# Performance work log

Measured on AMD Instinct MI355X. Metric: run time of the kernel, lower is better.

The kernel has to match this reference:

```python
import jax, jax.numpy as jnp
import numpy as np

B, S, H = 16, 2048, 1024

def setup_inputs() -> dict:
    key = jax.random.key(0)
    ks = jax.random.split(key, 6)
    return {
        "h": jax.random.normal(ks[0], (1, B, H), jnp.float32),
        "c": jax.random.normal(ks[1], (1, B, H), jnp.float32),
        "encoder_outputs": jax.random.normal(ks[2], (B, S, H), jnp.float32),
        "attn_W": jax.random.normal(ks[3], (H, 2 * H), jnp.float32) * 0.02,
        "attn_b": jax.random.normal(ks[4], (H,), jnp.float32) * 0.02,
        "v_W": jax.random.normal(ks[5], (1, H), jnp.float32) * 0.02,
    }

def reference(h, c, encoder_outputs, attn_W, attn_b, v_W):
    # h: (1,B,H) -> (B,1,H); a: (B,S,H)
    a = encoder_outputs
    hq = jnp.transpose(h, (1, 0, 2))  # (B,1,H)
    # cat((s, a), -1) @ attn_W.T == s @ Wh.T + a @ Wa.T (avoids (B,S,2H) buffer)
    Wh, Wa = attn_W[:, :H], attn_W[:, H:]
    energy = jax.nn.relu(
        jnp.einsum("bqh,oh->bqo", hq, Wh)          # (B,1,H), broadcast over S
        + jnp.einsum("bsh,oh->bso", a, Wa)
        + attn_b
    )  # (B,S,H)
    scores = jnp.einsum("bsh,h->bs", energy, v_W[0])  # (B,S)
    attn_weights = jax.nn.softmax(scores, axis=1)      # (B,S)
    context = jnp.einsum("bs,bsh->bh", attn_weights, a)[:, None, :]  # (B,1,H)
    return context, attn_weights
```

## Files before the change

kernel.cpp:

```cpp
#include <hip/hip_runtime.h>
#include <hip/hip_bf16.h>


typedef __bf16 bf16x8 __attribute__((ext_vector_type(8)));
typedef float floatx4 __attribute__((ext_vector_type(4)));

#define BB 16
#define SS 2048
#define HH 1024
#define MM (BB * SS)

#define GLB(p) ((const __attribute__((address_space(1))) void*)(p))
#define LDSP(p) ((__attribute__((address_space(3))) void*)(p))

__device__ inline ushort f2bf(float x) {
    uint32_t u = __builtin_bit_cast(uint32_t, x);
    u += 0x7FFFu + ((u >> 16) & 1u);
    return (ushort)(u >> 16);
}

__global__ __launch_bounds__(256) void convert_A_kernel(
    const float* __restrict__ src, __bf16* __restrict__ dst)
{
    size_t i = (size_t)blockIdx.x * 256 + threadIdx.x;
    const float* s = src + i * 8;
    float4 a = *(const float4*)(s);
    float4 b = *(const float4*)(s + 4);
    union { ushort u[8]; uint4 v; } p;
    p.u[0] = f2bf(a.x); p.u[1] = f2bf(a.y); p.u[2] = f2bf(a.z); p.u[3] = f2bf(a.w);
    p.u[4] = f2bf(b.x); p.u[5] = f2bf(b.y); p.u[6] = f2bf(b.z); p.u[7] = f2bf(b.w);
    *(uint4*)(dst + i * 8) = p.v;
}

__global__ __launch_bounds__(256) void prep_kernel(
    const float* __restrict__ h, const float* __restrict__ W,
    const float* __restrict__ bias, float* __restrict__ projh,
    __bf16* __restrict__ Wb, float* __restrict__ scores, float* __restrict__ ctx)
{
    int bid = blockIdx.x;
    int tid = threadIdx.x;
    if (bid < 256) {
        int b = bid >> 4;
        int oc = bid & 15;
        __shared__ float hrow[HH];
        *(float4*)&hrow[tid * 4] = *(const float4*)(h + (size_t)b * HH + tid * 4);
        __syncthreads();
        int ol = tid >> 2;
        int kq = tid & 3;
        int o = oc * 64 + ol;
        const float* wr = W + (size_t)o * (2 * HH) + kq * 256;
        const float* hb = hrow + kq * 256;
        float sum = 0.f;
        for (int k = 0; k < 256; k += 4) {
            float4 wv = *(const float4*)(wr + k);
            sum += hb[k] * wv.x + hb[k + 1] * wv.y + hb[k + 2] * wv.z + hb[k + 3] * wv.w;
        }
        sum += __shfl_xor(sum, 1);
        sum += __shfl_xor(sum, 2);
        if (kq == 0) projh[b * HH + o] = sum + bias[o];
    } else if (bid < 320) {
        int cb = bid - 256;
#pragma unroll
        for (int j = 0; j < 8; j++) {
            int g = cb * 2048 + tid + j * 256;
            int o = g >> 7;
            int k = (g & 127) * 8;
            const float* s = W + (size_t)o * (2 * HH) + HH + k;
            float4 a = *(const float4*)(s);
            float4 b2 = *(const float4*)(s + 4);
            union { ushort u[8]; uint4 v; } p;
            p.u[0] = f2bf(a.x); p.u[1] = f2bf(a.y); p.u[2] = f2bf(a.z); p.u[3] = f2bf(a.w);
            p.u[4] = f2bf(b2.x); p.u[5] = f2bf(b2.y); p.u[6] = f2bf(b2.z); p.u[7] = f2bf(b2.w);
            *(uint4*)(Wb + (size_t)o * HH + k) = p.v;
        }
    } else {
        int zb = bid - 320;
        float4 z = make_float4(0.f, 0.f, 0.f, 0.f);
        float* sp = scores + zb * 2048 + tid * 8;
        *(float4*)(sp) = z;
        *(float4*)(sp + 4) = z;
        *(float4*)(ctx + zb * 1024 + tid * 4) = z;
    }
}

__global__ __launch_bounds__(256) void gemm_scores_kernel(
    const __bf16* __restrict__ Ab,
    const __bf16* __restrict__ Wb,
    const float* __restrict__ projh,
    const float* __restrict__ vW,
    float* __restrict__ scores)
{
    constexpr int BM = 128, BN = 128, BK = 32;

    __shared__ __bf16 As[BM * BK];
    __shared__ __bf16 Bs[BN * BK];

    const int bid = blockIdx.x;
    const int grp = bid >> 6;
    const int r   = bid & 63;
    const int n0 = (r >> 3) * BN;
    const int my = grp * 8 + (r & 7);
    const int m0 = my * BM;
    const int bidx = m0 >> 11;

    const int tid = threadIdx.x;
    const int lane = tid & 63;
    const int wave = tid >> 6;
    const int wm = (wave & 1) * 64;
    const int wn = (wave >> 1) * 64;
    const int quad = lane >> 4;
    const int l16 = lane & 15;

    floatx4 acc[4][4];
    const floatx4 z = {0.f, 0.f, 0.f, 0.f};
#pragma unroll
    for (int i = 0; i < 4; i++)
#pragma unroll
        for (int j = 0; j < 4; j++) acc[i][j] = z;

    int g_row[4], g_col[4];
#pragma unroll
    for (int is = 0; is < 4; is++) {
        int part = is & 1;
        int c = part * 256 + tid;
        int u = c >> 3, j = c & 7;
        int jj = j ^ (u & 7);
        g_row[is] = u * 2 + (jj >> 2);
        g_col[is] = (jj & 3) * 8;
    }
    const __bf16* gA0 = Ab + (size_t)(m0 + g_row[0]) * HH + g_col[0];
    const __bf16* gA1 = Ab + (size_t)(m0 + g_row[1]) * HH + g_col[1];
    const __bf16* gB0 = Wb + (size_t)(n0 + g_row[2]) * HH + g_col[2];
    const __bf16* gB1 = Wb + (size_t)(n0 + g_row[3]) * HH + g_col[3];
    __bf16* lA0 = As + (size_t)wave * 512;
    __bf16* lA1 = As + 2048 + (size_t)wave * 512;
    __bf16* lB0 = Bs + (size_t)wave * 512;
    __bf16* lB1 = Bs + 2048 + (size_t)wave * 512;

    const __bf16* aaddr[4];
    const __bf16* baddr[4];
#pragma unroll
    for (int i = 0; i < 4; i++) {
        int frow = wm + i * 16 + l16;
        int u = frow >> 1;
        int cc = u * 8 + (((((frow & 1) << 2) | quad)) ^ (u & 7));
        aaddr[i] = &As[cc * 8];
        frow = wn + i * 16 + l16;
        u = frow >> 1;
        cc = u * 8 + (((((frow & 1) << 2) | quad)) ^ (u & 7));
        baddr[i] = &Bs[cc * 8];
    }

    for (int k0 = 0; k0 < HH; k0 += BK) {
        __syncthreads();
        __builtin_amdgcn_global_load_lds(GLB(gA0 + k0), LDSP(lA0), 16, 0, 0);
        __builtin_amdgcn_global_load_lds(GLB(gA1 + k0), LDSP(lA1), 16, 0, 0);
        __builtin_amdgcn_global_load_lds(GLB(gB0 + k0), LDSP(lB0), 16, 0, 0);
        __builtin_amdgcn_global_load_lds(GLB(gB1 + k0), LDSP(lB1), 16, 0, 0);
        __syncthreads();

        bf16x8 af[4], bf[4];
#pragma unroll
        for (int i = 0; i < 4; i++) af[i] = *(const bf16x8*)aaddr[i];
#pragma unroll
        for (int j = 0; j < 4; j++) bf[j] = *(const bf16x8*)baddr[j];
#pragma unroll
        for (int i = 0; i < 4; i++)
#pragma unroll
            for (int j = 0; j < 4; j++)
                acc[i][j] = __builtin_amdgcn_mfma_f32_16x16x32_bf16(af[i], bf[j], acc[i][j], 0, 0, 0);
    }

    float ph[4], vv[4];
#pragma unroll
    for (int j = 0; j < 4; j++) {
        int ng = n0 + wn + j * 16 + l16;
        ph[j] = projh[bidx * HH + ng];
        vv[j] = vW[ng];
    }
#pragma unroll
    for (int i = 0; i < 4; i++) {
        float s[4] = {0.f, 0.f, 0.f, 0.f};
#pragma unroll
        for (int j = 0; j < 4; j++) {
#pragma unroll
            for (int r2 = 0; r2 < 4; r2++) {
                float e = acc[i][j][r2] + ph[j];
                e = e > 0.f ? e : 0.f;
                s[r2] += e * vv[j];
            }
        }
#pragma unroll
        for (int r2 = 0; r2 < 4; r2++) {
            s[r2] += __shfl_xor(s[r2], 1);
            s[r2] += __shfl_xor(s[r2], 2);
            s[r2] += __shfl_xor(s[r2], 4);
            s[r2] += __shfl_xor(s[r2], 8);
        }
        if (l16 == 0) {
#pragma unroll
            for (int r2 = 0; r2 < 4; r2++) {
                int mg = m0 + wm + i * 16 + quad * 4 + r2;
                atomicAdd(&scores[mg], s[r2]);
            }
        }
    }
}

__global__ __launch_bounds__(256) void gemm_scores_f32_kernel(
    const float* __restrict__ A, const float* __restrict__ W,
    const float* __restrict__ projh, const float* __restrict__ vW,
    float* __restrict__ scores)
{
    constexpr int BM = 128, BN = 128, BK = 32, LDT = BK + 8;
    __shared__ __bf16 As[BM * LDT];
    __shared__ __bf16 Bs[BN * LDT];
    const int n0 = blockIdx.x * BN;
    const int m0 = blockIdx.y * BM;
    const int bidx = m0 >> 11;
    const int tid = threadIdx.x;
    const int lane = tid & 63;
    const int wave = tid >> 6;
    const int wm = (wave & 1) * 64;
    const int wn = (wave >> 1) * 64;
    const int quad = lane >> 4;
    const int l16 = lane & 15;
    floatx4 acc[4][4];
    const floatx4 z = {0.f, 0.f, 0.f, 0.f};
#pragma unroll
    for (int i = 0; i < 4; i++)
#pragma unroll
        for (int j = 0; j < 4; j++) acc[i][j] = z;
    int rowT[4], colT[4];
#pragma unroll
    for (int i = 0; i < 4; i++) {
        int fi = tid + 256 * i;
        rowT[i] = fi >> 3;
        colT[i] = (fi & 7) * 4;
    }
    for (int k0 = 0; k0 < HH; k0 += BK) {
        float4 av[4], bv[4];
#pragma unroll
        for (int i = 0; i < 4; i++) {
            av[i] = *(const float4*)(A + (size_t)(m0 + rowT[i]) * HH + k0 + colT[i]);
            bv[i] = *(const float4*)(W + (size_t)(n0 + rowT[i]) * (2 * HH) + HH + k0 + colT[i]);
        }
        __syncthreads();
#pragma unroll
        for (int i = 0; i < 4; i++) {
            ushort4 ua = make_ushort4(f2bf(av[i].x), f2bf(av[i].y), f2bf(av[i].z), f2bf(av[i].w));
            ushort4 ub = make_ushort4(f2bf(bv[i].x), f2bf(bv[i].y), f2bf(bv[i].z), f2bf(bv[i].w));
            *(ushort4*)&As[rowT[i] * LDT + colT[i]] = ua;
            *(ushort4*)&Bs[rowT[i] * LDT + colT[i]] = ub;
        }
        __syncthreads();
        bf16x8 af[4], bf[4];
#pragma unroll
        for (int i = 0; i < 4; i++)
            af[i] = *(const bf16x8*)&As[(wm + i * 16 + l16) * LDT + quad * 8];
#pragma unroll
        for (int j = 0; j < 4; j++)
            bf[j] = *(const bf16x8*)&Bs[(wn + j * 16 + l16) * LDT + quad * 8];
#pragma unroll
        for (int i = 0; i < 4; i++)
#pragma unroll
            for (int j = 0; j < 4; j++)
                acc[i][j] = __builtin_amdgcn_mfma_f32_16x16x32_bf16(af[i], bf[j], acc[i][j], 0, 0, 0);
    }
    float ph[4], vv[4];
#pragma unroll
    for (int j = 0; j < 4; j++) {
        int ng = n0 + wn + j * 16 + l16;
        ph[j] = projh[bidx * HH + ng];
        vv[j] = vW[ng];
    }
#pragma unroll
    for (int i = 0; i < 4; i++) {
        float s[4] = {0.f, 0.f, 0.f, 0.f};
#pragma unroll
        for (int j = 0; j < 4; j++) {
#pragma unroll
            for (int r = 0; r < 4; r++) {
                float e = acc[i][j][r] + ph[j];
                e = e > 0.f ? e : 0.f;
                s[r] += e * vv[j];
            }
        }
#pragma unroll
        for (int r = 0; r < 4; r++) {
            s[r] += __shfl_xor(s[r], 1);
            s[r] += __shfl_xor(s[r], 2);
            s[r] += __shfl_xor(s[r], 4);
            s[r] += __shfl_xor(s[r], 8);
        }
        if (l16 == 0) {
#pragma unroll
            for (int r = 0; r < 4; r++) {
                int mg = m0 + wm + i * 16 + quad * 4 + r;
                atomicAdd(&scores[mg], s[r]);
            }
        }
    }
}

__global__ __launch_bounds__(256) void softmax_kernel(
    const float* __restrict__ scores, float* __restrict__ wout)
{
    int b = blockIdx.x;
    int tid = threadIdx.x;
    const float* row = scores + b * SS;
    float x[8];
    float mx = -1e30f;
#pragma unroll
    for (int i = 0; i < 8; i++) { x[i] = row[tid + i * 256]; mx = fmaxf(mx, x[i]); }
#pragma unroll
    for (int off = 32; off; off >>= 1) mx = fmaxf(mx, __shfl_xor(mx, off));
    __shared__ float redm[4], reds[4];
    if ((tid & 63) == 0) redm[tid >> 6] = mx;
    __syncthreads();
    mx = fmaxf(fmaxf(redm[0], redm[1]), fmaxf(redm[2], redm[3]));
    float sum = 0.f;
#pragma unroll
    for (int i = 0; i < 8; i++) { x[i] = __expf(x[i] - mx); sum += x[i]; }
#pragma unroll
    for (int off = 32; off; off >>= 1) sum += __shfl_xor(sum, off);
    if ((tid & 63) == 0) reds[tid >> 6] = sum;
    __syncthreads();
    float inv = 1.0f / (reds[0] + reds[1] + reds[2] + reds[3]);
#pragma unroll
    for (int i = 0; i < 8; i++) wout[b * SS + tid + i * 256] = x[i] * inv;
}

__global__ __launch_bounds__(256) void context_kernel(
    const float* __restrict__ A, const float* __restrict__ wgt, float* __restrict__ ctx)
{
    int b = blockIdx.x >> 4;
    int sc = blockIdx.x & 15;
    int tid = threadIdx.x;
    const float* arow = A + ((size_t)b * SS + sc * 128) * HH + tid * 4;
    const float* wrow = wgt + b * SS + sc * 128;
    float4 acc = make_float4(0.f, 0.f, 0.f, 0.f);
#pragma unroll 4
    for (int s = 0; s < 128; s++) {
        float w = wrow[s];
        float4 v = *(const float4*)(arow + (size_t)s * HH);
        acc.x += w * v.x; acc.y += w * v.y; acc.z += w * v.z; acc.w += w * v.w;
    }
    float* o = ctx + b * HH + tid * 4;
    atomicAdd(o + 0, acc.x);
    atomicAdd(o + 1, acc.y);
    atomicAdd(o + 2, acc.z);
    atomicAdd(o + 3, acc.w);
}

extern "C" void kernel_launch(void* const* d_in, const int* in_sizes, int n_in,
                              void* d_out, int out_size, void* d_ws, size_t ws_size,
                              hipStream_t stream) {
    const float* h    = (const float*)d_in[0];
    const float* a    = (const float*)d_in[2];
    const float* W    = (const float*)d_in[3];
    const float* bias = (const float*)d_in[4];
    const float* vW   = (const float*)d_in[5];
    float* out = (float*)d_out;

    float* projh  = (float*)d_ws;
    float* scores = projh + BB * HH;
    __bf16* Wb = (__bf16*)(scores + MM);
    __bf16* Ab = Wb + (size_t)HH * HH;
    const size_t need = (size_t)(BB * HH + MM) * 4 + (size_t)HH * HH * 2
                      + (size_t)MM * HH * 2;

    if (ws_size >= need) {
        prep_kernel<<<336, 256, 0, stream>>>(h, W, bias, projh, Wb, scores, out);
        convert_A_kernel<<<(MM * HH / 8) / 256, 256, 0, stream>>>(a, Ab);
        gemm_scores_kernel<<<2048, 256, 0, stream>>>(Ab, Wb, projh, vW, scores);
    } else {
        prep_kernel<<<336, 256, 0, stream>>>(h, W, bias, projh, Wb, scores, out);
        gemm_scores_f32_kernel<<<dim3(HH / 128, MM / 128), 256, 0, stream>>>(a, W, projh, vW, scores);
    }

    softmax_kernel<<<BB, 256, 0, stream>>>(scores, out + BB * HH);
    context_kernel<<<BB * 16, 256, 0, stream>>>(a, out + BB * HH, out);
}
```

Measured before the change: 323.7 us.

## Load GEMM fragments directly from global with register double buffering

The bf16 GEMM no longer stages tiles through LDS with global_load_lds and two barriers per K step. Each wave now loads its MFMA fragments straight from global memory into registers, prefetching the next K slice into a second register buffer, and the launch bounds request 3 blocks per SU. The context kernel is also split into 64-row chunks over twice as many blocks, for more parallelism at the cost of more atomics. Dropping LDS removes reuse across waves, so each A/B row is fetched by two waves through cache, and the 16-byte per-lane loads at stride HH are poorly coalesced.

```diff
diff --git a/kernel.cpp b/kernel.cpp
--- a/kernel.cpp
+++ b/kernel.cpp
@@ -9,9 +9,6 @@
 #define SS 2048
 #define HH 1024
 #define MM (BB * SS)
-
-#define GLB(p) ((const __attribute__((address_space(1))) void*)(p))
-#define LDSP(p) ((__attribute__((address_space(3))) void*)(p))
 
 __device__ inline ushort f2bf(float x) {
     uint32_t u = __builtin_bit_cast(uint32_t, x);
@@ -83,17 +80,14 @@
     }
 }
 
-__global__ __launch_bounds__(256) void gemm_scores_kernel(
+__global__ __launch_bounds__(256, 3) void gemm_scores_kernel(
     const __bf16* __restrict__ Ab,
     const __bf16* __restrict__ Wb,
     const float* __restrict__ projh,
     const float* __restrict__ vW,
     float* __restrict__ scores)
 {
-    constexpr int BM = 128, BN = 128, BK = 32;
-
-    __shared__ __bf16 As[BM * BK];
-    __shared__ __bf16 Bs[BN * BK];
+    constexpr int BM = 128, BN = 128;
 
     const int bid = blockIdx.x;
     const int grp = bid >> 6;
@@ -118,57 +112,34 @@
 #pragma unroll
         for (int j = 0; j < 4; j++) acc[i][j] = z;
 
-    int g_row[4], g_col[4];
-#pragma unroll
-    for (int is = 0; is < 4; is++) {
-        int part = is & 1;
-        int c = part * 256 + tid;
-        int u = c >> 3, j = c & 7;
-        int jj = j ^ (u & 7);
-        g_row[is] = u * 2 + (jj >> 2);
-        g_col[is] = (jj & 3) * 8;
-    }
-    const __bf16* gA0 = Ab + (size_t)(m0 + g_row[0]) * HH + g_col[0];
-    const __bf16* gA1 = Ab + (size_t)(m0 + g_row[1]) * HH + g_col[1];
-    const __bf16* gB0 = Wb + (size_t)(n0 + g_row[2]) * HH + g_col[2];
-    const __bf16* gB1 = Wb + (size_t)(n0 + g_row[3]) * HH + g_col[3];
-    __bf16* lA0 = As + (size_t)wave * 512;
-    __bf16* lA1 = As + 2048 + (size_t)wave * 512;
-    __bf16* lB0 = Bs + (size_t)wave * 512;
-    __bf16* lB1 = Bs + 2048 + (size_t)wave * 512;
-
-    const __bf16* aaddr[4];
-    const __bf16* baddr[4];
-#pragma unroll
-    for (int i = 0; i < 4; i++) {
-        int frow = wm + i * 16 + l16;
-        int u = frow >> 1;
-        int cc = u * 8 + (((((frow & 1) << 2) | quad)) ^ (u & 7));
-        aaddr[i] = &As[cc * 8];
-        frow = wn + i * 16 + l16;
-        u = frow >> 1;
-        cc = u * 8 + (((((frow & 1) << 2) | quad)) ^ (u & 7));
-        baddr[i] = &Bs[cc * 8];
-    }
-
-    for (int k0 = 0; k0 < HH; k0 += BK) {
-        __syncthreads();
-        __builtin_amdgcn_global_load_lds(GLB(gA0 + k0), LDSP(lA0), 16, 0, 0);
-        __builtin_amdgcn_global_load_lds(GLB(gA1 + k0), LDSP(lA1), 16, 0, 0);
-        __builtin_amdgcn_global_load_lds(GLB(gB0 + k0), LDSP(lB0), 16, 0, 0);
-        __builtin_amdgcn_global_load_lds(GLB(gB1 + k0), LDSP(lB1), 16, 0, 0);
-        __syncthreads();
-
-        bf16x8 af[4], bf[4];
-#pragma unroll
-        for (int i = 0; i < 4; i++) af[i] = *(const bf16x8*)aaddr[i];
-#pragma unroll
-        for (int j = 0; j < 4; j++) bf[j] = *(const bf16x8*)baddr[j];
+    const __bf16* aptr[4];
+    const __bf16* bptr[4];
+#pragma unroll
+    for (int i = 0; i < 4; i++) {
+        aptr[i] = Ab + (size_t)(m0 + wm + i * 16 + l16) * HH + quad * 8;
+        bptr[i] = Wb + (size_t)(n0 + wn + i * 16 + l16) * HH + quad * 8;
+    }
+
+    bf16x8 af[2][4], bf[2][4];
+#pragma unroll
+    for (int i = 0; i < 4; i++) {
+        af[0][i] = *(const bf16x8*)(aptr[i]);
+        bf[0][i] = *(const bf16x8*)(bptr[i]);
+    }
+
+    int buf = 0;
+    for (int k0 = 0; k0 < HH; k0 += 32, buf ^= 1) {
+        int kn = (k0 + 32) & (HH - 1);
+#pragma unroll
+        for (int i = 0; i < 4; i++) {
+            af[buf ^ 1][i] = *(const bf16x8*)(aptr[i] + kn);
+            bf[buf ^ 1][i] = *(const bf16x8*)(bptr[i] + kn);
+        }
 #pragma unroll
         for (int i = 0; i < 4; i++)
 #pragma unroll
             for (int j = 0; j < 4; j++)
-                acc[i][j] = __builtin_amdgcn_mfma_f32_16x16x32_bf16(af[i], bf[j], acc[i][j], 0, 0, 0);
+                acc[i][j] = __builtin_amdgcn_mfma_f32_16x16x32_bf16(af[buf][i], bf[buf][j], acc[i][j], 0, 0, 0);
     }
 
     float ph[4], vv[4];
@@ -334,14 +305,14 @@
 __global__ __launch_bounds__(256) void context_kernel(
     const float* __restrict__ A, const float* __restrict__ wgt, float* __restrict__ ctx)
 {
-    int b = blockIdx.x >> 4;
-    int sc = blockIdx.x & 15;
+    int b = blockIdx.x >> 5;
+    int sc = blockIdx.x & 31;
     int tid = threadIdx.x;
-    const float* arow = A + ((size_t)b * SS + sc * 128) * HH + tid * 4;
-    const float* wrow = wgt + b * SS + sc * 128;
+    const float* arow = A + ((size_t)b * SS + sc * 64) * HH + tid * 4;
+    const float* wrow = wgt + b * SS + sc * 64;
     float4 acc = make_float4(0.f, 0.f, 0.f, 0.f);
 #pragma unroll 4
-    for (int s = 0; s < 128; s++) {
+    for (int s = 0; s < 64; s++) {
         float w = wrow[s];
         float4 v = *(const float4*)(arow + (size_t)s * HH);
         acc.x += w * v.x; acc.y += w * v.y; acc.z += w * v.z; acc.w += w * v.w;
@@ -380,5 +351,5 @@
     }
 
     softmax_kernel<<<BB, 256, 0, stream>>>(scores, out + BB * HH);
-    context_kernel<<<BB * 16, 256, 0, stream>>>(a, out + BB * HH, out);
-}
+    context_kernel<<<BB * 32, 256, 0, stream>>>(a, out + BB * HH, out);
+}
```

Result: slower. 506.3 us (+56.4%).
